# Optimization experiments

Measured on AMD Instinct MI355X. Metric: run time of the kernel, lower is better.

## Reference

```python
import math
import jax, jax.numpy as jnp
import numpy as np

PI_APPROX = 3.1415926  # the module's hard-coded pi in KVal


def _factratio(N, D):
    # python-float replica of PRT.factratio
    if N >= D:
        p = 1.0
        for i in range(D + 1, N + 1):
            p *= i
        return p
    p = 1.0
    for i in range(N + 1, D + 1):
        p *= i
    return 1.0 / p


def _kval(M, L):
    return math.sqrt((2 * L + 1) / (4 * PI_APPROX) * _factratio(L - M, L + M))


def _assoc_legendre(M, L, x):
    # x = cos(theta), |x| <= 1 by construction so the zero-guard branch never fires
    pmm = jnp.ones_like(x)
    if M > 0:
        somx2 = jnp.sqrt((1.0 + x) * (1.0 - x))
        fact = 1.0
        for _ in range(1, M + 1):
            pmm = -pmm * fact * somx2
            fact = fact + 2
    if L == M:
        return pmm
    pmmp1 = x * (2 * M + 1) * pmm
    if L == M + 1:
        return pmmp1
    pll = pmmp1
    for i in range(M + 2, L + 1):
        pll = (x * (2 * i - 1) * pmmp1 - (i + M - 1) * pmm) / (i - M)
        pmm, pmmp1 = pmmp1, pll
    return pll


def _spherical_harmonic(M, L, theta, phi):
    sqrt2 = math.sqrt(2.0)
    ct = jnp.cos(theta)
    if M > 0:
        return sqrt2 * _kval(M, L) * jnp.cos(M * phi) * _assoc_legendre(M, L, ct)
    elif M < 0:
        return sqrt2 * _kval(-M, L) * jnp.sin(-M * phi) * _assoc_legendre(-M, L, ct)
    else:
        return _kval(0, L) * _assoc_legendre(0, L, ct)


def _sh_coeffs(order, phi, theta):
    # [N_rays, S, (order+1)^2] -- loop is over the small fixed harmonic index set
    shs = [_spherical_harmonic(m, l, theta, phi)
           for l in range(order + 1) for m in range(-l, l + 1)]
    return jnp.stack(shs, axis=-1)


def setup_inputs() -> dict:
    key = jax.random.key(0)
    k1, k2, k3 = jax.random.split(key, 3)
    N_RAYS, N, ORDER = 32768, 16, 3
    S = N * N
    xv = jax.random.uniform(k1, (N_RAYS, S), dtype=jnp.float32)
    yv = jax.random.uniform(k2, (N_RAYS, S), dtype=jnp.float32)
    theta = jnp.arccos(1.0 - 2.0 * xv)          # matches sampleSphericalDirections_N_rays
    phi = (2.0 * math.pi) * yv
    # binary visibility per sphere sample
    p_vis = (jax.random.uniform(k3, (N_RAYS, S, 1), dtype=jnp.float32) > 0.5).astype(jnp.float32)
    return {"p_vis": p_vis, "phi": phi, "theta": theta, "n": N, "order": ORDER}


def reference(p_vis, phi, theta, n, order):
    sh = _sh_coeffs(order, phi, theta)           # [R, S, K]
    w = 4.0 * math.pi / (n * n)                   # module uses math.pi here
    prt = jnp.sum(sh * p_vis, axis=1)             # [R, K]
    return jnp.clip(prt * w, -2.0, 2.0)
```

## Files before the change

kernel.cpp:

```cpp
#include <hip/hip_runtime.h>
#include <math.h>


__global__ __launch_bounds__(256) void prt_kernel(
    const float* __restrict__ vis,
    const float* __restrict__ phi,
    const float* __restrict__ theta,
    const int* __restrict__ n_ptr,
    float* __restrict__ out,
    int n_rays)
{
    const int lane = threadIdx.x & 63;
    const int gwv  = (blockIdx.x * 256 + threadIdx.x) >> 6;
    const int ray0 = gwv * 4;
    if (ray0 >= n_rays) return;

    const int g = lane >> 4;
    const int t = lane & 15;
    const int sbase = (ray0 + g) * 256 + t * 4;

    float4 ph[4], th[4], vv[4];
    #pragma unroll
    for (int j = 0; j < 4; ++j) {
        const int a = sbase + 64 * j;
        ph[j] = *reinterpret_cast<const float4*>(phi + a);
        th[j] = *reinterpret_cast<const float4*>(theta + a);
        vv[j] = *reinterpret_cast<const float4*>(vis + a);
    }

    float acc[16];
    #pragma unroll
    for (int i = 0; i < 16; ++i) acc[i] = 0.0f;

    #pragma unroll
    for (int j = 0; j < 4; ++j) {
        const float* phs = reinterpret_cast<const float*>(&ph[j]);
        const float* ths = reinterpret_cast<const float*>(&th[j]);
        const float* vvs = reinterpret_cast<const float*>(&vv[j]);
        #pragma unroll
        for (int e = 0; e < 4; ++e) {
            float s, x;
            __sincosf(ths[e], &s, &x);
            float sp, cp;
            __sincosf(phs[e], &sp, &cp);

            const float sq = s * s;
            const float s2 = 2.0f * sp * cp;
            const float c2 = fmaf(-2.0f * sp, sp, 1.0f);
            const float s3 = fmaf(s2, cp, c2 * sp);
            const float c3 = fmaf(-s2, sp, c2 * cp);

            const float v    = vvs[e];
            const float t1   = v * s;
            const float vx   = v * x;
            const float t2   = vx * s;
            const float vsq  = v * sq;
            const float vxsq = vx * sq;
            const float vsqs = vsq * s;

            const float x2  = x * x;
            const float P20 = fmaf(1.5f, x2, -0.5f);
            const float q1  = fmaf(5.0f, x2, -1.0f);
            const float r30 = fmaf(2.5f, x2, -1.5f);
            const float t1q = t1 * q1;

            acc[0]  += v;
            acc[1]   = fmaf(t1,   sp,  acc[1]);
            acc[2]  += vx;
            acc[3]   = fmaf(t1,   cp,  acc[3]);
            acc[4]   = fmaf(vsq,  s2,  acc[4]);
            acc[5]   = fmaf(t2,   sp,  acc[5]);
            acc[6]   = fmaf(v,    P20, acc[6]);
            acc[7]   = fmaf(t2,   cp,  acc[7]);
            acc[8]   = fmaf(vsq,  c2,  acc[8]);
            acc[9]   = fmaf(vsqs, s3,  acc[9]);
            acc[10]  = fmaf(vxsq, s2,  acc[10]);
            acc[11]  = fmaf(t1q,  sp,  acc[11]);
            acc[12]  = fmaf(vx,   r30, acc[12]);
            acc[13]  = fmaf(t1q,  cp,  acc[13]);
            acc[14]  = fmaf(vxsq, c2,  acc[14]);
            acc[15]  = fmaf(vsqs, c3,  acc[15]);
        }
    }

    const bool b0 = (lane & 1) != 0;
    const bool b1 = (lane & 2) != 0;
    const bool b2 = (lane & 4) != 0;
    const bool b3 = (lane & 8) != 0;

    #pragma unroll
    for (int j = 0; j < 8; ++j) {
        const float a0 = acc[2 * j], a1 = acc[2 * j + 1];
        const float keep = b0 ? a1 : a0;
        const float give = b0 ? a0 : a1;
        acc[j] = keep + __shfl_xor(give, 1, 64);
    }
    #pragma unroll
    for (int j = 0; j < 4; ++j) {
        const float a0 = acc[2 * j], a1 = acc[2 * j + 1];
        const float keep = b1 ? a1 : a0;
        const float give = b1 ? a0 : a1;
        acc[j] = keep + __shfl_xor(give, 2, 64);
    }
    #pragma unroll
    for (int j = 0; j < 2; ++j) {
        const float a0 = acc[2 * j], a1 = acc[2 * j + 1];
        const float keep = b2 ? a1 : a0;
        const float give = b2 ? a0 : a1;
        acc[j] = keep + __shfl_xor(give, 4, 64);
    }
    float r;
    {
        const float keep = b3 ? acc[1] : acc[0];
        const float give = b3 ? acc[0] : acc[1];
        r = keep + __shfl_xor(give, 8, 64);
    }

    const float k01   = b0 ? -0.48860253f : 0.28209481f;
    const float k23   = b0 ? -0.48860253f : 0.48860253f;
    const float k45   = b0 ? -1.09254847f : 0.54627424f;
    const float k67   = b0 ? -1.09254847f : 0.63078316f;
    const float k89   = b0 ? -0.59004360f : 0.54627424f;
    const float k1011 = b0 ? -0.45704580f : 1.44530571f;
    const float k1213 = b0 ? -0.45704580f : 0.74635269f;
    const float k1415 = b0 ? -0.59004360f : 1.44530571f;
    const float ka = b1 ? k23 : k01;
    const float kb = b1 ? k67 : k45;
    const float kc = b1 ? k1011 : k89;
    const float kd = b1 ? k1415 : k1213;
    const float ke = b2 ? kb : ka;
    const float kf = b2 ? kd : kc;
    const float K  = b3 ? kf : ke;

    const int n = *n_ptr;
    const float w = 12.566370614359172f / (float)(n * n);

    const float res = fminf(fmaxf(r * K * w, -2.0f), 2.0f);

    out[ray0 * 16 + lane] = res;
}

extern "C" void kernel_launch(void* const* d_in, const int* in_sizes, int n_in,
                              void* d_out, int out_size, void* d_ws, size_t ws_size,
                              hipStream_t stream) {
    const float* vis   = (const float*)d_in[0];
    const float* phi   = (const float*)d_in[1];
    const float* theta = (const float*)d_in[2];
    const int*   n_ptr = (const int*)d_in[3];

    float* out = (float*)d_out;

    const int n_rays = in_sizes[1] / 256;
    const int rays_per_block = 16;
    const int blocks = (n_rays + rays_per_block - 1) / rays_per_block;
    prt_kernel<<<blocks, 256, 0, stream>>>(vis, phi, theta, n_ptr, out, n_rays);
}
```

Measured before the change: 119.3 us.

## Process four ray tiles per wave with double-buffered register prefetch

Each wave now handles four 4-ray tiles in a grid-stride pattern instead of one. Loads for the next tile are issued into a second register buffer before computing the current one, so memory latency overlaps with the sincos and FMA work. This cuts the grid to a quarter of its former block count and roughly doubles live registers for input data. That may lower occupancy and leave fewer waves per CU to hide latency.

```diff
diff --git a/kernel.cpp b/kernel.cpp
--- a/kernel.cpp
+++ b/kernel.cpp
@@ -1,6 +1,10 @@
 #include <hip/hip_runtime.h>
 #include <math.h>
 
+
+struct Tile {
+    float4 ph[4], th[4], vv[4];
+};
 
 __global__ __launch_bounds__(256) void prt_kernel(
     const float* __restrict__ vis,
@@ -11,110 +15,16 @@
     int n_rays)
 {
     const int lane = threadIdx.x & 63;
-    const int gwv  = (blockIdx.x * 256 + threadIdx.x) >> 6;
-    const int ray0 = gwv * 4;
-    if (ray0 >= n_rays) return;
-
-    const int g = lane >> 4;
-    const int t = lane & 15;
-    const int sbase = (ray0 + g) * 256 + t * 4;
-
-    float4 ph[4], th[4], vv[4];
-    #pragma unroll
-    for (int j = 0; j < 4; ++j) {
-        const int a = sbase + 64 * j;
-        ph[j] = *reinterpret_cast<const float4*>(phi + a);
-        th[j] = *reinterpret_cast<const float4*>(theta + a);
-        vv[j] = *reinterpret_cast<const float4*>(vis + a);
-    }
-
-    float acc[16];
-    #pragma unroll
-    for (int i = 0; i < 16; ++i) acc[i] = 0.0f;
-
-    #pragma unroll
-    for (int j = 0; j < 4; ++j) {
-        const float* phs = reinterpret_cast<const float*>(&ph[j]);
-        const float* ths = reinterpret_cast<const float*>(&th[j]);
-        const float* vvs = reinterpret_cast<const float*>(&vv[j]);
-        #pragma unroll
-        for (int e = 0; e < 4; ++e) {
-            float s, x;
-            __sincosf(ths[e], &s, &x);
-            float sp, cp;
-            __sincosf(phs[e], &sp, &cp);
-
-            const float sq = s * s;
-            const float s2 = 2.0f * sp * cp;
-            const float c2 = fmaf(-2.0f * sp, sp, 1.0f);
-            const float s3 = fmaf(s2, cp, c2 * sp);
-            const float c3 = fmaf(-s2, sp, c2 * cp);
-
-            const float v    = vvs[e];
-            const float t1   = v * s;
-            const float vx   = v * x;
-            const float t2   = vx * s;
-            const float vsq  = v * sq;
-            const float vxsq = vx * sq;
-            const float vsqs = vsq * s;
-
-            const float x2  = x * x;
-            const float P20 = fmaf(1.5f, x2, -0.5f);
-            const float q1  = fmaf(5.0f, x2, -1.0f);
-            const float r30 = fmaf(2.5f, x2, -1.5f);
-            const float t1q = t1 * q1;
-
-            acc[0]  += v;
-            acc[1]   = fmaf(t1,   sp,  acc[1]);
-            acc[2]  += vx;
-            acc[3]   = fmaf(t1,   cp,  acc[3]);
-            acc[4]   = fmaf(vsq,  s2,  acc[4]);
-            acc[5]   = fmaf(t2,   sp,  acc[5]);
-            acc[6]   = fmaf(v,    P20, acc[6]);
-            acc[7]   = fmaf(t2,   cp,  acc[7]);
-            acc[8]   = fmaf(vsq,  c2,  acc[8]);
-            acc[9]   = fmaf(vsqs, s3,  acc[9]);
-            acc[10]  = fmaf(vxsq, s2,  acc[10]);
-            acc[11]  = fmaf(t1q,  sp,  acc[11]);
-            acc[12]  = fmaf(vx,   r30, acc[12]);
-            acc[13]  = fmaf(t1q,  cp,  acc[13]);
-            acc[14]  = fmaf(vxsq, c2,  acc[14]);
-            acc[15]  = fmaf(vsqs, c3,  acc[15]);
-        }
-    }
+    const int wv   = (blockIdx.x * 256 + threadIdx.x) >> 6;
+    const int NW   = gridDim.x << 2;
+    const int g    = lane >> 4;
+    const int t    = lane & 15;
+    const int ntiles = n_rays >> 2;
 
     const bool b0 = (lane & 1) != 0;
     const bool b1 = (lane & 2) != 0;
     const bool b2 = (lane & 4) != 0;
     const bool b3 = (lane & 8) != 0;
-
-    #pragma unroll
-    for (int j = 0; j < 8; ++j) {
-        const float a0 = acc[2 * j], a1 = acc[2 * j + 1];
-        const float keep = b0 ? a1 : a0;
-        const float give = b0 ? a0 : a1;
-        acc[j] = keep + __shfl_xor(give, 1, 64);
-    }
-    #pragma unroll
-    for (int j = 0; j < 4; ++j) {
-        const float a0 = acc[2 * j], a1 = acc[2 * j + 1];
-        const float keep = b1 ? a1 : a0;
-        const float give = b1 ? a0 : a1;
-        acc[j] = keep + __shfl_xor(give, 2, 64);
-    }
-    #pragma unroll
-    for (int j = 0; j < 2; ++j) {
-        const float a0 = acc[2 * j], a1 = acc[2 * j + 1];
-        const float keep = b2 ? a1 : a0;
-        const float give = b2 ? a0 : a1;
-        acc[j] = keep + __shfl_xor(give, 4, 64);
-    }
-    float r;
-    {
-        const float keep = b3 ? acc[1] : acc[0];
-        const float give = b3 ? acc[0] : acc[1];
-        r = keep + __shfl_xor(give, 8, 64);
-    }
 
     const float k01   = b0 ? -0.48860253f : 0.28209481f;
     const float k23   = b0 ? -0.48860253f : 0.48860253f;
@@ -135,9 +45,119 @@
     const int n = *n_ptr;
     const float w = 12.566370614359172f / (float)(n * n);
 
-    const float res = fminf(fmaxf(r * K * w, -2.0f), 2.0f);
+    auto load_tile = [&](Tile& T, int tile) {
+        const int sbase = (tile * 4 + g) * 256 + t * 4;
+        #pragma unroll
+        for (int j = 0; j < 4; ++j) {
+            const int a = sbase + 64 * j;
+            T.ph[j] = *reinterpret_cast<const float4*>(phi + a);
+            T.th[j] = *reinterpret_cast<const float4*>(theta + a);
+            T.vv[j] = *reinterpret_cast<const float4*>(vis + a);
+        }
+    };
 
-    out[ray0 * 16 + lane] = res;
+    auto compute_store = [&](const Tile& T, int tile) {
+        float acc[16];
+        #pragma unroll
+        for (int i = 0; i < 16; ++i) acc[i] = 0.0f;
+
+        #pragma unroll
+        for (int j = 0; j < 4; ++j) {
+            const float* phs = reinterpret_cast<const float*>(&T.ph[j]);
+            const float* ths = reinterpret_cast<const float*>(&T.th[j]);
+            const float* vvs = reinterpret_cast<const float*>(&T.vv[j]);
+            #pragma unroll
+            for (int e = 0; e < 4; ++e) {
+                float s, x;
+                __sincosf(ths[e], &s, &x);
+                float sp, cp;
+                __sincosf(phs[e], &sp, &cp);
+
+                const float sq = s * s;
+                const float s2 = 2.0f * sp * cp;
+                const float c2 = fmaf(-2.0f * sp, sp, 1.0f);
+                const float s3 = fmaf(s2, cp, c2 * sp);
+                const float c3 = fmaf(-s2, sp, c2 * cp);
+
+                const float v    = vvs[e];
+                const float t1   = v * s;
+                const float vx   = v * x;
+                const float t2   = vx * s;
+                const float vsq  = v * sq;
+                const float vxsq = vx * sq;
+                const float vsqs = vsq * s;
+
+                const float x2  = x * x;
+                const float P20 = fmaf(1.5f, x2, -0.5f);
+                const float q1  = fmaf(5.0f, x2, -1.0f);
+                const float r30 = fmaf(2.5f, x2, -1.5f);
+                const float t1q = t1 * q1;
+
+                acc[0]  += v;
+                acc[1]   = fmaf(t1,   sp,  acc[1]);
+                acc[2]  += vx;
+                acc[3]   = fmaf(t1,   cp,  acc[3]);
+                acc[4]   = fmaf(vsq,  s2,  acc[4]);
+                acc[5]   = fmaf(t2,   sp,  acc[5]);
+                acc[6]   = fmaf(v,    P20, acc[6]);
+                acc[7]   = fmaf(t2,   cp,  acc[7]);
+                acc[8]   = fmaf(vsq,  c2,  acc[8]);
+                acc[9]   = fmaf(vsqs, s3,  acc[9]);
+                acc[10]  = fmaf(vxsq, s2,  acc[10]);
+                acc[11]  = fmaf(t1q,  sp,  acc[11]);
+                acc[12]  = fmaf(vx,   r30, acc[12]);
+                acc[13]  = fmaf(t1q,  cp,  acc[13]);
+                acc[14]  = fmaf(vxsq, c2,  acc[14]);
+                acc[15]  = fmaf(vsqs, c3,  acc[15]);
+            }
+        }
+
+        #pragma unroll
+        for (int j = 0; j < 8; ++j) {
+            const float a0 = acc[2 * j], a1 = acc[2 * j + 1];
+            const float keep = b0 ? a1 : a0;
+            const float give = b0 ? a0 : a1;
+            acc[j] = keep + __shfl_xor(give, 1, 64);
+        }
+        #pragma unroll
+        for (int j = 0; j < 4; ++j) {
+            const float a0 = acc[2 * j], a1 = acc[2 * j + 1];
+            const float keep = b1 ? a1 : a0;
+            const float give = b1 ? a0 : a1;
+            acc[j] = keep + __shfl_xor(give, 2, 64);
+        }
+        #pragma unroll
+        for (int j = 0; j < 2; ++j) {
+            const float a0 = acc[2 * j], a1 = acc[2 * j + 1];
+            const float keep = b2 ? a1 : a0;
+            const float give = b2 ? a0 : a1;
+            acc[j] = keep + __shfl_xor(give, 4, 64);
+        }
+        float r;
+        {
+            const float keep = b3 ? acc[1] : acc[0];
+            const float give = b3 ? acc[0] : acc[1];
+            r = keep + __shfl_xor(give, 8, 64);
+        }
+
+        const float res = fminf(fmaxf(r * K * w, -2.0f), 2.0f);
+        out[tile * 64 + lane] = res;
+    };
+
+    const int t0 = wv;
+    const int t1 = wv + NW;
+    const int t2 = wv + 2 * NW;
+    const int t3 = wv + 3 * NW;
+
+    Tile A, B;
+    if (t0 < ntiles) load_tile(A, t0);
+    if (t1 < ntiles) load_tile(B, t1);
+    if (t0 < ntiles) compute_store(A, t0);
+    if (t2 < ntiles) load_tile(A, t2);
+    if (t1 < ntiles) compute_store(B, t1);
+    if (t3 < ntiles) load_tile(B, t3);
+    if (t2 < ntiles) compute_store(A, t2);
+    if (t3 < ntiles) compute_store(B, t3);
 }
 
 extern "C" void kernel_launch(void* const* d_in, const int* in_sizes, int n_in,
@@ -151,7 +171,7 @@
     float* out = (float*)d_out;
 
     const int n_rays = in_sizes[1] / 256;
-    const int rays_per_block = 16;
-    const int blocks = (n_rays + rays_per_block - 1) / rays_per_block;
+    const int ntiles = n_rays / 4;
+    const int blocks = (ntiles + 15) / 16;
     prt_kernel<<<blocks, 256, 0, stream>>>(vis, phi, theta, n_ptr, out, n_rays);
 }
```

Result: no change. 121.4 us (+1.7%).
